# Optimization experiments

Hardware: AMD Instinct MI355X
Metric: run time of the kernel (lower is better)

Reference implementation:

```python
import jax, jax.numpy as jnp
import numpy as np

E = 8        # num_experts
K = 2        # top_k
B, S, D, H = 4, 2048, 1024, 2048  # batch, seq, input_size, hidden_size (GLU -> 2H fan-out)


def act_quant(x):
    # per-token 8-bit absmax quantization (BitNet style)
    scale = 127.0 / jnp.clip(jnp.max(jnp.abs(x), axis=-1, keepdims=True), 1e-5)
    return jnp.clip(jnp.round(x * scale), -128, 127) / scale


def weight_quant(w):
    # per-(expert)-tensor 1.58-bit quantization to {-1,0,1}/scale
    scale = 1.0 / jnp.clip(jnp.mean(jnp.abs(w)), 1e-5)
    return jnp.clip(jnp.round(w * scale), -1, 1) / scale


def ste(x, q):
    # straight-through estimator: forward uses q, backward passes grad of x
    return x + jax.lax.stop_gradient(q - x)


def setup_inputs() -> dict:
    key = jax.random.key(0)
    k0, k1, k2, k3 = jax.random.split(key, 4)
    x = jax.random.normal(k0, (B, S, D), jnp.float32)
    w_gate = jax.random.normal(k1, (D, E), jnp.float32) * 0.02   # router (no bias)
    w_in = jax.random.normal(k2, (E, 2 * H, D), jnp.float32) * 0.02   # ParallelExperts1_58b input_linear [E, out, in]
    w_out = jax.random.normal(k3, (E, D, H), jnp.float32) * 0.02      # output_linear [E, out, in]
    bias = jnp.zeros((D,), jnp.float32)
    return {"x": x, "w_gate": w_gate, "w_in": w_in, "w_out": w_out, "bias": bias}


def reference(x, w_gate, w_in, w_out, bias):
    bsz, length, d = x.shape
    xf = x.reshape(-1, d)                               # [N, D]
    logits = xf @ w_gate                                # [N, E]
    top_logits, top_idx = jax.lax.top_k(logits, K)      # [N, K]
    gates = jax.nn.softmax(top_logits, axis=-1)         # [N, K]

    # load-balancing aux loss (switch loss + z-loss), training-mode router loss
    probs = jax.nn.softmax(logits, axis=-1)
    onehot = jax.nn.one_hot(top_idx, E, dtype=logits.dtype).sum(axis=1)  # [N, E]
    freq = onehot.sum(axis=0)
    p = probs.sum(axis=0)
    switchloss = E * jnp.sum((p / jnp.sum(p)) * (freq / jnp.sum(freq)))
    zloss = jnp.sum(jax.nn.logsumexp(logits, axis=-1) ** 2) / xf.shape[0]
    loss = switchloss + 0.1 * zloss

    # STE-quantized activations and per-expert ternary weights
    xq = ste(xf, act_quant(xf))                          # [N, D]
    win_q = jax.vmap(lambda w: ste(w, weight_quant(w)))(w_in)    # [E, 2H, D]
    wout_q = jax.vmap(lambda w: ste(w, weight_quant(w)))(w_out)  # [E, D, H]

    # dense expert loop (E is small/static); gates zero-out non-routed tokens,
    # equivalent to the gather/grouped-GEMM/index_add pipeline in the original.
    y = jnp.zeros_like(xf)
    for e in range(E):
        gate_e = jnp.sum(jnp.where(top_idx == e, gates, 0.0), axis=1)  # [N]
        h = xq @ win_q[e].T                              # [N, 2H]
        h1, g = jnp.split(h, 2, axis=-1)
        h = jax.nn.silu(h1) * g                          # GLU
        hq = ste(h, act_quant(h))
        y = y + gate_e[:, None] * (hq @ wout_q[e].T)     # [N, D]

    y = y.reshape(bsz, length, d) + bias
    return y, loss
```

## Files before the change

kernel.cpp:

```cpp
#include <hip/hip_runtime.h>
#include <math.h>

typedef __attribute__((ext_vector_type(4))) int   i32x4;
typedef __attribute__((ext_vector_type(4))) float f32x4;
typedef __attribute__((ext_vector_type(8))) unsigned short u16x8;

#define NTOK   8192
#define DIMD   1024
#define HID    2048
#define NEXP   8
#define NPAIR  16384

#define XQ_OFF      0L
#define WQIN_OFF    8388608L
#define WQOUT_OFF   41943040L
#define HQ_OFF      58720256L
#define GLU_OFF     92274688L
#define XREC_OFF    226492416L
#define GATE_OFF    226525184L
#define HREC_OFF    226590720L
#define HABS_OFF    226656256L
#define TLIST_OFF   226721792L
#define CNT_OFF     226983936L
#define PSUM_OFF    226983968L
#define ZSUM_OFF    226984000L
#define PART_OFF    226984032L
#define WRECIN_OFF  226988128L
#define WRECOUT_OFF 226988160L
#define WSCLIN_OFF  226988192L
#define WSCLOUT_OFF 226988224L

__device__ __forceinline__ int clampi(int v, int lo, int hi){ return v<lo?lo:(v>hi?hi:v); }

__device__ __forceinline__ unsigned packq(f32x4 v, float s, int lo, int hi){
  int q0 = clampi((int)rintf(v.x*s), lo, hi);
  int q1 = clampi((int)rintf(v.y*s), lo, hi);
  int q2 = clampi((int)rintf(v.z*s), lo, hi);
  int q3 = clampi((int)rintf(v.w*s), lo, hi);
  return (unsigned)((q0&255)|((q1&255)<<8)|((q2&255)<<16)|((q3&255)<<24));
}

__device__ __forceinline__ unsigned short f2bf(float f){
  unsigned u = __float_as_uint(f);
  u += 0x7fffu + ((u >> 16) & 1u);
  return (unsigned short)(u >> 16);
}
__device__ __forceinline__ float bf2f(unsigned short b){
  return __uint_as_float(((unsigned)b) << 16);
}

__global__ void k_init(unsigned* __restrict__ habs, int* __restrict__ cnts,
                       float* __restrict__ psum, float* __restrict__ zsum){
  int i = blockIdx.x*blockDim.x + threadIdx.x;
  if (i < NPAIR) habs[i] = 0u;
  if (i < 8){ cnts[i]=0; psum[i]=0.f; }
  if (i == 8) zsum[0]=0.f;
}

__global__ __launch_bounds__(1024) void k_router(
    const float* __restrict__ x, const float* __restrict__ wg,
    signed char* __restrict__ xq, float* __restrict__ xrec,
    float* __restrict__ gatep, int* __restrict__ tlist, int* __restrict__ cnts,
    float* __restrict__ psum, float* __restrict__ zsum)
{
  __shared__ float ls_p[8]; __shared__ float ls_z[1];
  __shared__ int ls_c[8];  __shared__ int ls_b[8];
  int tid = threadIdx.x;
  if (tid<8){ ls_p[tid]=0.f; ls_c[tid]=0; }
  if (tid==8) ls_z[0]=0.f;
  __syncthreads();
  int wave = tid>>6, lane = tid&63;
  int tok = blockIdx.x*16 + wave;

  const f32x4* x4 = (const f32x4*)(x + (long)tok*DIMD) + lane*4;
  f32x4 xv[4];
  #pragma unroll
  for (int j=0;j<4;++j) xv[j] = x4[j];

  float amax = 0.f;
  float lg[8] = {0,0,0,0,0,0,0,0};
  const f32x4* wg4 = (const f32x4*)wg;
  #pragma unroll
  for (int j=0;j<16;++j){
    float xd = xv[j>>2][j&3];
    amax = fmaxf(amax, fabsf(xd));
    int d = lane*16 + j;
    f32x4 w0 = wg4[d*2], w1 = wg4[d*2+1];
    lg[0]+=xd*w0.x; lg[1]+=xd*w0.y; lg[2]+=xd*w0.z; lg[3]+=xd*w0.w;
    lg[4]+=xd*w1.x; lg[5]+=xd*w1.y; lg[6]+=xd*w1.z; lg[7]+=xd*w1.w;
  }
  for (int m=1;m<64;m<<=1){
    amax = fmaxf(amax, __shfl_xor(amax, m));
    #pragma unroll
    for (int e=0;e<8;++e) lg[e] += __shfl_xor(lg[e], m);
  }
  float cm = fmaxf(amax, 1e-5f);
  float sx = 127.f/cm;
  unsigned p0 = packq(xv[0], sx, -128, 127);
  unsigned p1 = packq(xv[1], sx, -128, 127);
  unsigned p2 = packq(xv[2], sx, -128, 127);
  unsigned p3 = packq(xv[3], sx, -128, 127);
  i32x4 pk; pk.x=(int)p0; pk.y=(int)p1; pk.z=(int)p2; pk.w=(int)p3;
  *(i32x4*)(xq + (long)tok*DIMD + lane*16) = pk;

  int e1=0, e2=0, s1=0, s2=0;
  if (lane==0){
    xrec[tok] = cm*(1.f/127.f);
    e1 = 0;
    for (int e=1;e<8;++e) if (lg[e] > lg[e1]) e1 = e;
    e2 = (e1==0)?1:0;
    for (int e=0;e<8;++e) if (e!=e1 && lg[e] > lg[e2]) e2 = e;
    float t = expf(lg[e2]-lg[e1]);
    gatep[tok*2]   = 1.f/(1.f+t);
    gatep[tok*2+1] = t/(1.f+t);
    float mx = lg[e1], sum = 0.f, pr[8];
    #pragma unroll
    for (int e=0;e<8;++e){ pr[e] = expf(lg[e]-mx); sum += pr[e]; }
    float inv = 1.f/sum;
    #pragma unroll
    for (int e=0;e<8;++e) atomicAdd(&ls_p[e], pr[e]*inv);
    float lse = mx + logf(sum);
    atomicAdd(&ls_z[0], lse*lse);
    s1 = atomicAdd(&ls_c[e1], 1);
    s2 = atomicAdd(&ls_c[e2], 1);
  }
  __syncthreads();
  if (tid<8) ls_b[tid] = atomicAdd(&cnts[tid], ls_c[tid]);
  __syncthreads();
  if (lane==0){
    tlist[e1*NTOK + ls_b[e1] + s1] = tok*2;
    tlist[e2*NTOK + ls_b[e2] + s2] = tok*2 + 1;
  }
  if (tid<8)  atomicAdd(&psum[tid], ls_p[tid]);
  if (tid==8) atomicAdd(zsum, ls_z[0]);
}

__global__ void k_wabs(const float* __restrict__ w_in, const float* __restrict__ w_out,
                       float* __restrict__ part){
  int b = blockIdx.x, tid = threadIdx.x;
  const float* base = (b < 512) ? (w_in + (long)b*65536) : (w_out + (long)(b-512)*65536);
  const f32x4* p4 = (const f32x4*)base;
  float s = 0.f;
  for (int i = tid; i < 16384; i += 256){
    f32x4 v = p4[i];
    s += fabsf(v.x)+fabsf(v.y)+fabsf(v.z)+fabsf(v.w);
  }
  __shared__ float red[256];
  red[tid] = s; __syncthreads();
  for (int off=128; off; off>>=1){ if (tid<off) red[tid]+=red[tid+off]; __syncthreads(); }
  if (tid==0) part[b] = red[0];
}

__global__ void k_wmean(const float* __restrict__ part,
                        float* __restrict__ wrec_in, float* __restrict__ wrec_out,
                        float* __restrict__ wscl_in, float* __restrict__ wscl_out){
  int t = threadIdx.x;
  if (t < 8){
    float s = 0.f;
    for (int i=0;i<64;++i) s += part[t*64+i];
    float cmm = fmaxf(s/4194304.f, 1e-5f);
    wrec_in[t] = cmm; wscl_in[t] = 1.f/cmm;
  } else if (t < 16){
    int e = t-8; float s = 0.f;
    for (int i=0;i<32;++i) s += part[512 + e*32 + i];
    float cmm = fmaxf(s/2097152.f, 1e-5f);
    wrec_out[e] = cmm; wscl_out[e] = 1.f/cmm;
  }
}

__global__ void k_packw(const float* __restrict__ w, i32x4* __restrict__ wq,
                        const float* __restrict__ wscl, int COLS, int K, int KB,
                        long chunksPerE){
  long t = (long)blockIdx.x*blockDim.x + threadIdx.x;
  int e = (int)(t / chunksPerE);
  long r = t - (long)e*chunksPerE;
  int lane = (int)(r & 63);
  long fb = r >> 6;
  int kb = (int)(fb % KB);
  int cb = (int)(fb / KB);
  int col = cb*16 + (lane & 15);
  int k0  = kb*64 + (lane >> 4)*16;
  const f32x4* src = (const f32x4*)(w + ((long)e*COLS + col)*K + k0);
  float s = wscl[e];
  f32x4 v0 = src[0], v1 = src[1], v2 = src[2], v3 = src[3];
  i32x4 o;
  o.x = (int)packq(v0, s, -1, 1);
  o.y = (int)packq(v1, s, -1, 1);
  o.z = (int)packq(v2, s, -1, 1);
  o.w = (int)packq(v3, s, -1, 1);
  wq[t] = o;
}

#define MFMA8(A, B, ACC) \
  { _Pragma("unroll") for (int c=0;c<8;++c) \
      ACC[c] = __builtin_amdgcn_mfma_i32_16x16x64_i8(A, B[c], ACC[c], 0,0,0); }

__global__ __launch_bounds__(256) void k_gemm1(
    const signed char* __restrict__ xq, const signed char* __restrict__ wqin,
    const int* __restrict__ tlist, const int* __restrict__ cnts,
    const float* __restrict__ xrec, const float* __restrict__ wrec_in,
    unsigned short* __restrict__ glu, unsigned* __restrict__ habs)
{
  const int e = blockIdx.y;
  const int cnt = cnts[e];
  const int slot = blockIdx.x >> 5;
  const int row0 = slot << 7;
  if (row0 >= cnt) return;
  const int ctile = blockIdx.x & 31;
  const int wave = threadIdx.x >> 6, lane = threadIdx.x & 63;
  const int l15 = lane & 15, lhi = lane >> 4;
  const int rbase = row0 + wave*32;
  const int* tl = tlist + e*NTOK;

  const i32x4* aptr[2];
  #pragma unroll
  for (int rt=0; rt<2; ++rt){
    int r = rbase + rt*16 + l15;
    int pr = tl[min(r, cnt-1)];
    aptr[rt] = (const i32x4*)(xq + (long)(pr>>1)*DIMD + lhi*16);
  }
  const i32x4* bbase[8];
  {
    const signed char* wp = wqin + (long)e*4194304 + (long)lane*16;
    #pragma unroll
    for (int c=0;c<8;++c){
      int cb_c = (c<4) ? (ctile*4 + c) : (128 + ctile*4 + (c-4));
      bbase[c] = (const i32x4*)(wp + (long)cb_c*16384);
    }
  }
  i32x4 acc0[8] = {}, acc1[8] = {};
  i32x4 e_a0 = aptr[0][0],  e_a1 = aptr[1][0];
  i32x4 o_a0 = aptr[0][4],  o_a1 = aptr[1][4];
  i32x4 e_b[8], o_b[8];
  #pragma unroll
  for (int c=0;c<8;++c){ e_b[c] = bbase[c][0]; o_b[c] = bbase[c][64]; }
  #pragma unroll 1
  for (int kb=0; kb<14; kb+=2){
    MFMA8(e_a0, e_b, acc0); MFMA8(e_a1, e_b, acc1);
    e_a0 = aptr[0][(kb+2)*4]; e_a1 = aptr[1][(kb+2)*4];
    #pragma unroll
    for (int c=0;c<8;++c) e_b[c] = bbase[c][(kb+2)*64];
    MFMA8(o_a0, o_b, acc0); MFMA8(o_a1, o_b, acc1);
    o_a0 = aptr[0][(kb+3)*4]; o_a1 = aptr[1][(kb+3)*4];
    #pragma unroll
    for (int c=0;c<8;++c) o_b[c] = bbase[c][(kb+3)*64];
  }
  MFMA8(e_a0, e_b, acc0); MFMA8(e_a1, e_b, acc1);
  MFMA8(o_a0, o_b, acc0); MFMA8(o_a1, o_b, acc1);

  const float wr = wrec_in[e];
  #pragma unroll
  for (int rt=0; rt<2; ++rt){
    #pragma unroll
    for (int i=0; i<4; ++i){
      int r = rbase + rt*16 + lhi*4 + i;
      bool valid = (r < cnt);
      int pr = valid ? tl[r] : 0;
      float dq = xrec[pr>>1] * wr;
      float m = 0.f;
      #pragma unroll
      for (int c=0;c<4;++c){
        float h1 = (float)(rt==0 ? acc0[c][i]   : acc1[c][i])   * dq;
        float gg = (float)(rt==0 ? acc0[c+4][i] : acc1[c+4][i]) * dq;
        float sil = h1 / (1.f + expf(-h1));
        float v = sil * gg;
        m = fmaxf(m, fabsf(v));
        if (valid) glu[(long)pr*HID + ctile*64 + c*16 + l15] = f2bf(v);
      }
      #pragma unroll
      for (int mm=1; mm<16; mm<<=1) m = fmaxf(m, __shfl_xor(m, mm));
      if (valid && l15==0) atomicMax(habs + pr, __float_as_uint(m));
    }
  }
}

__global__ void k_quanth(const unsigned short* __restrict__ glu, const unsigned* __restrict__ habs,
                         signed char* __restrict__ hq, float* __restrict__ hrec){
  int p = blockIdx.x, t = threadIdx.x;
  float am = __uint_as_float(habs[p]);
  float cmm = fmaxf(am, 1e-5f);
  if (t==0) hrec[p] = cmm*(1.f/127.f);
  float s = 127.f/cmm;
  u16x8 v = ((const u16x8*)(glu + (long)p*HID))[t];
  f32x4 f0, f1;
  f0.x=bf2f(v[0]); f0.y=bf2f(v[1]); f0.z=bf2f(v[2]); f0.w=bf2f(v[3]);
  f1.x=bf2f(v[4]); f1.y=bf2f(v[5]); f1.z=bf2f(v[6]); f1.w=bf2f(v[7]);
  uint2 u; u.x = packq(f0, s, -128, 127); u.y = packq(f1, s, -128, 127);
  ((uint2*)(hq + (long)p*HID))[t] = u;
}

__global__ __launch_bounds__(256) void k_gemm2(
    const signed char* __restrict__ hq, const signed char* __restrict__ wqout,
    const int* __restrict__ tlist, const int* __restrict__ cnts,
    const float* __restrict__ hrec, const float* __restrict__ gatep,
    const float* __restrict__ wrec_out, float* __restrict__ pout)
{
  const int e = blockIdx.y;
  const int cnt = cnts[e];
  const int slot = blockIdx.x >> 3;
  const int row0 = slot << 7;
  if (row0 >= cnt) return;
  const int ctile = blockIdx.x & 7;
  const int dcol0 = ctile*128;
  const int wave = threadIdx.x >> 6, lane = threadIdx.x & 63;
  const int l15 = lane & 15, lhi = lane >> 4;
  const int rbase = row0 + wave*32;
  const int* tl = tlist + e*NTOK;

  const i32x4* aptr[2];
  #pragma unroll
  for (int rt=0; rt<2; ++rt){
    int r = rbase + rt*16 + l15;
    int pr = tl[min(r, cnt-1)];
    aptr[rt] = (const i32x4*)(hq + (long)pr*HID + lhi*16);
  }
  const i32x4* bbase[8];
  {
    const signed char* wp = wqout + (long)e*2097152 + (long)lane*16;
    #pragma unroll
    for (int c=0;c<8;++c){
      int cb_c = ctile*8 + c;
      bbase[c] = (const i32x4*)(wp + (long)cb_c*32768);
    }
  }
  i32x4 acc0[8] = {}, acc1[8] = {};
  i32x4 e_a0 = aptr[0][0],  e_a1 = aptr[1][0];
  i32x4 o_a0 = aptr[0][4],  o_a1 = aptr[1][4];
  i32x4 e_b[8], o_b[8];
  #pragma unroll
  for (int c=0;c<8;++c){ e_b[c] = bbase[c][0]; o_b[c] = bbase[c][64]; }
  #pragma unroll 1
  for (int kb=0; kb<30; kb+=2){
    MFMA8(e_a0, e_b, acc0); MFMA8(e_a1, e_b, acc1);
    e_a0 = aptr[0][(kb+2)*4]; e_a1 = aptr[1][(kb+2)*4];
    #pragma unroll
    for (int c=0;c<8;++c) e_b[c] = bbase[c][(kb+2)*64];
    MFMA8(o_a0, o_b, acc0); MFMA8(o_a1, o_b, acc1);
    o_a0 = aptr[0][(kb+3)*4]; o_a1 = aptr[1][(kb+3)*4];
    #pragma unroll
    for (int c=0;c<8;++c) o_b[c] = bbase[c][(kb+3)*64];
  }
  MFMA8(e_a0, e_b, acc0); MFMA8(e_a1, e_b, acc1);
  MFMA8(o_a0, o_b, acc0); MFMA8(o_a1, o_b, acc1);

  const float wr = wrec_out[e];
  #pragma unroll
  for (int rt=0; rt<2; ++rt){
    #pragma unroll
    for (int i=0; i<4; ++i){
      int r = rbase + rt*16 + lhi*4 + i;
      if (r >= cnt) continue;
      int pr = tl[r];
      float f = gatep[pr] * hrec[pr] * wr;
      #pragma unroll
      for (int c=0;c<8;++c)
        pout[(long)pr*DIMD + dcol0 + c*16 + l15] = (float)(rt==0 ? acc0[c][i] : acc1[c][i]) * f;
    }
  }
}

__global__ void k_combine(const float* __restrict__ pout, const float* __restrict__ bias,
                          float* __restrict__ y){
  long idx = (long)blockIdx.x*blockDim.x + threadIdx.x;
  int tok = (int)(idx >> 8);
  int c4  = (int)(idx & 255);
  f32x4 b  = ((const f32x4*)bias)[c4];
  const f32x4* p = (const f32x4*)(pout + (long)tok*2*DIMD);
  f32x4 r = b + p[c4] + p[256 + c4];
  ((f32x4*)(y + (long)tok*DIMD))[c4] = r;
}

__global__ void k_loss(const int* __restrict__ cnts, const float* __restrict__ psum,
                       const float* __restrict__ zsum, float* __restrict__ out){
  if (threadIdx.x==0 && blockIdx.x==0){
    float sp=0.f, sf=0.f, sw=0.f;
    for (int e=0;e<8;++e){
      float f = (float)cnts[e];
      sp += psum[e]; sf += f; sw += psum[e]*f;
    }
    float loss = 8.f*sw/(sp*sf) + 0.1f*zsum[0]/(float)NTOK;
    out[(long)NTOK*DIMD] = loss;
  }
}

extern "C" void kernel_launch(void* const* d_in, const int* in_sizes, int n_in,
                              void* d_out, int out_size, void* d_ws, size_t ws_size,
                              hipStream_t stream){
  const float* x     = (const float*)d_in[0];
  const float* wg    = (const float*)d_in[1];
  const float* w_in  = (const float*)d_in[2];
  const float* w_out = (const float*)d_in[3];
  const float* bias  = (const float*)d_in[4];
  float* y = (float*)d_out;
  char* ws = (char*)d_ws;

  signed char* xq    = (signed char*)(ws + XQ_OFF);
  signed char* wqin  = (signed char*)(ws + WQIN_OFF);
  signed char* wqout = (signed char*)(ws + WQOUT_OFF);
  signed char* hq    = (signed char*)(ws + HQ_OFF);
  unsigned short* glu = (unsigned short*)(ws + GLU_OFF);
  float* pout  = (float*)(ws + GLU_OFF);
  float* xrec  = (float*)(ws + XREC_OFF);
  float* gatep = (float*)(ws + GATE_OFF);
  float* hrec  = (float*)(ws + HREC_OFF);
  unsigned* habs = (unsigned*)(ws + HABS_OFF);
  int* tlist = (int*)(ws + TLIST_OFF);
  int* cnts  = (int*)(ws + CNT_OFF);
  float* psum = (float*)(ws + PSUM_OFF);
  float* zsum = (float*)(ws + ZSUM_OFF);
  float* part = (float*)(ws + PART_OFF);
  float* wrec_in  = (float*)(ws + WRECIN_OFF);
  float* wrec_out = (float*)(ws + WRECOUT_OFF);
  float* wscl_in  = (float*)(ws + WSCLIN_OFF);
  float* wscl_out = (float*)(ws + WSCLOUT_OFF);

  k_init  <<<64, 256, 0, stream>>>(habs, cnts, psum, zsum);
  k_router<<<512, 1024, 0, stream>>>(x, wg, xq, xrec, gatep, tlist, cnts, psum, zsum);
  k_wabs  <<<768, 256, 0, stream>>>(w_in, w_out, part);
  k_wmean <<<1, 64, 0, stream>>>(part, wrec_in, wrec_out, wscl_in, wscl_out);
  k_packw <<<8192, 256, 0, stream>>>(w_in,  (i32x4*)wqin,  wscl_in,  4096, 1024, 16, 262144L);
  k_packw <<<4096, 256, 0, stream>>>(w_out, (i32x4*)wqout, wscl_out, 1024, 2048, 32, 131072L);
  k_gemm1 <<<dim3(2048, 8), 256, 0, stream>>>(xq, wqin, tlist, cnts, xrec, wrec_in, glu, habs);
  k_quanth<<<NPAIR, 256, 0, stream>>>(glu, habs, hq, hrec);
  k_gemm2 <<<dim3(512, 8), 256, 0, stream>>>(hq, wqout, tlist, cnts, hrec, gatep, wrec_out, pout);
  k_combine<<<8192, 256, 0, stream>>>(pout, bias, y);
  k_loss  <<<1, 64, 0, stream>>>(cnts, psum, zsum, y);
}
```

Baseline: 479.2 us.

## Switch expert GEMMs to 32x32x32 int8 MFMA with grid-stride job scheduling

Replaces the 16x16x64 int8 MFMA tiles in both expert GEMMs with 32x32x32 int8 MFMA using four 16-wide accumulators per wave. The weight packing layout changes to match the new operand fragment shape. Both GEMMs move from a 2D grid with many early-exit blocks to a persistent-style 1D grid where each block loops over jobs interleaved across experts. The goal is higher MFMA throughput per instruction, fewer redundant operand loads, and less launch waste from empty tiles. The epilogue is reworked for the new accumulator row mapping, including a wider shuffle reduction for the row absmax.

```diff
diff --git a/kernel.cpp b/kernel.cpp
--- a/kernel.cpp
+++ b/kernel.cpp
@@ -1,9 +1,10 @@
 #include <hip/hip_runtime.h>
 #include <math.h>
 
-typedef __attribute__((ext_vector_type(4))) int   i32x4;
-typedef __attribute__((ext_vector_type(4))) float f32x4;
-typedef __attribute__((ext_vector_type(8))) unsigned short u16x8;
+typedef __attribute__((ext_vector_type(4)))  int   i32x4;
+typedef __attribute__((ext_vector_type(16))) int   i32x16;
+typedef __attribute__((ext_vector_type(4)))  float f32x4;
+typedef __attribute__((ext_vector_type(8)))  unsigned short u16x8;
 
 #define NTOK   8192
 #define DIMD   1024
@@ -178,8 +179,8 @@
   long fb = r >> 6;
   int kb = (int)(fb % KB);
   int cb = (int)(fb / KB);
-  int col = cb*16 + (lane & 15);
-  int k0  = kb*64 + (lane >> 4)*16;
+  int col = cb*32 + (lane & 31);
+  int k0  = kb*32 + (lane >> 5)*16;
   const f32x4* src = (const f32x4*)(w + ((long)e*COLS + col)*K + k0);
   float s = wscl[e];
   f32x4 v0 = src[0], v1 = src[1], v2 = src[2], v3 = src[3];
@@ -191,9 +192,11 @@
   wq[t] = o;
 }
 
-#define MFMA8(A, B, ACC) \
-  { _Pragma("unroll") for (int c=0;c<8;++c) \
-      ACC[c] = __builtin_amdgcn_mfma_i32_16x16x64_i8(A, B[c], ACC[c], 0,0,0); }
+#define MFMA32(A, B0, B1, B2, B3) \
+  acc0 = __builtin_amdgcn_mfma_i32_32x32x32_i8(A, B0, acc0, 0,0,0); \
+  acc1 = __builtin_amdgcn_mfma_i32_32x32x32_i8(A, B1, acc1, 0,0,0); \
+  acc2 = __builtin_amdgcn_mfma_i32_32x32x32_i8(A, B2, acc2, 0,0,0); \
+  acc3 = __builtin_amdgcn_mfma_i32_32x32x32_i8(A, B3, acc3, 0,0,0);
 
 __global__ __launch_bounds__(256) void k_gemm1(
     const signed char* __restrict__ xq, const signed char* __restrict__ wqin,
@@ -201,75 +204,64 @@
     const float* __restrict__ xrec, const float* __restrict__ wrec_in,
     unsigned short* __restrict__ glu, unsigned* __restrict__ habs)
 {
-  const int e = blockIdx.y;
-  const int cnt = cnts[e];
-  const int slot = blockIdx.x >> 5;
-  const int row0 = slot << 7;
-  if (row0 >= cnt) return;
-  const int ctile = blockIdx.x & 31;
   const int wave = threadIdx.x >> 6, lane = threadIdx.x & 63;
-  const int l15 = lane & 15, lhi = lane >> 4;
-  const int rbase = row0 + wave*32;
-  const int* tl = tlist + e*NTOK;
-
-  const i32x4* aptr[2];
-  #pragma unroll
-  for (int rt=0; rt<2; ++rt){
-    int r = rbase + rt*16 + l15;
-    int pr = tl[min(r, cnt-1)];
-    aptr[rt] = (const i32x4*)(xq + (long)(pr>>1)*DIMD + lhi*16);
-  }
-  const i32x4* bbase[8];
-  {
+  const int l31 = lane & 31, lhi = lane >> 5;
+  for (int job = blockIdx.x; job < 16384; job += 4096){
+    const int ctile = job & 31;
+    const int e = (job >> 5) & 7;
+    const int slot = job >> 8;
+    const int cnt = cnts[e];
+    const int row0 = slot << 7;
+    if (row0 >= cnt) continue;
+
+    const int* tl = tlist + e*NTOK;
+    const int rbase = row0 + wave*32;
+    const int ar = tl[min(rbase + l31, cnt-1)];
+    const i32x4* ap = (const i32x4*)(xq + (long)(ar>>1)*DIMD + lhi*16);
     const signed char* wp = wqin + (long)e*4194304 + (long)lane*16;
+    const i32x4* bp0 = (const i32x4*)(wp + (long)(ctile*2     )*32768);
+    const i32x4* bp1 = (const i32x4*)(wp + (long)(ctile*2 +  1)*32768);
+    const i32x4* bp2 = (const i32x4*)(wp + (long)(ctile*2 + 64)*32768);
+    const i32x4* bp3 = (const i32x4*)(wp + (long)(ctile*2 + 65)*32768);
+
+    i32x16 acc0 = (i32x16)0, acc1 = (i32x16)0, acc2 = (i32x16)0, acc3 = (i32x16)0;
+    i32x4 ea = ap[0], oa = ap[2];
+    i32x4 eb0 = bp0[0],  eb1 = bp1[0],  eb2 = bp2[0],  eb3 = bp3[0];
+    i32x4 ob0 = bp0[64], ob1 = bp1[64], ob2 = bp2[64], ob3 = bp3[64];
+    #pragma unroll 1
+    for (int kb=0; kb<30; kb+=2){
+      ap += 4; bp0 += 128; bp1 += 128; bp2 += 128; bp3 += 128;
+      MFMA32(ea, eb0, eb1, eb2, eb3);
+      ea = ap[0];
+      eb0 = bp0[0]; eb1 = bp1[0]; eb2 = bp2[0]; eb3 = bp3[0];
+      MFMA32(oa, ob0, ob1, ob2, ob3);
+      oa = ap[2];
+      ob0 = bp0[64]; ob1 = bp1[64]; ob2 = bp2[64]; ob3 = bp3[64];
+    }
+    MFMA32(ea, eb0, eb1, eb2, eb3);
+    MFMA32(oa, ob0, ob1, ob2, ob3);
+
+    const float wr = wrec_in[e];
     #pragma unroll
-    for (int c=0;c<8;++c){
-      int cb_c = (c<4) ? (ctile*4 + c) : (128 + ctile*4 + (c-4));
-      bbase[c] = (const i32x4*)(wp + (long)cb_c*16384);
-    }
-  }
-  i32x4 acc0[8] = {}, acc1[8] = {};
-  i32x4 e_a0 = aptr[0][0],  e_a1 = aptr[1][0];
-  i32x4 o_a0 = aptr[0][4],  o_a1 = aptr[1][4];
-  i32x4 e_b[8], o_b[8];
-  #pragma unroll
-  for (int c=0;c<8;++c){ e_b[c] = bbase[c][0]; o_b[c] = bbase[c][64]; }
-  #pragma unroll 1
-  for (int kb=0; kb<14; kb+=2){
-    MFMA8(e_a0, e_b, acc0); MFMA8(e_a1, e_b, acc1);
-    e_a0 = aptr[0][(kb+2)*4]; e_a1 = aptr[1][(kb+2)*4];
-    #pragma unroll
-    for (int c=0;c<8;++c) e_b[c] = bbase[c][(kb+2)*64];
-    MFMA8(o_a0, o_b, acc0); MFMA8(o_a1, o_b, acc1);
-    o_a0 = aptr[0][(kb+3)*4]; o_a1 = aptr[1][(kb+3)*4];
-    #pragma unroll
-    for (int c=0;c<8;++c) o_b[c] = bbase[c][(kb+3)*64];
-  }
-  MFMA8(e_a0, e_b, acc0); MFMA8(e_a1, e_b, acc1);
-  MFMA8(o_a0, o_b, acc0); MFMA8(o_a1, o_b, acc1);
-
-  const float wr = wrec_in[e];
-  #pragma unroll
-  for (int rt=0; rt<2; ++rt){
-    #pragma unroll
-    for (int i=0; i<4; ++i){
-      int r = rbase + rt*16 + lhi*4 + i;
+    for (int g=0; g<16; ++g){
+      int rl = (g&3) + 8*(g>>2) + 4*lhi;
+      int r  = rbase + rl;
       bool valid = (r < cnt);
       int pr = valid ? tl[r] : 0;
       float dq = xrec[pr>>1] * wr;
-      float m = 0.f;
-      #pragma unroll
-      for (int c=0;c<4;++c){
-        float h1 = (float)(rt==0 ? acc0[c][i]   : acc1[c][i])   * dq;
-        float gg = (float)(rt==0 ? acc0[c+4][i] : acc1[c+4][i]) * dq;
-        float sil = h1 / (1.f + expf(-h1));
-        float v = sil * gg;
-        m = fmaxf(m, fabsf(v));
-        if (valid) glu[(long)pr*HID + ctile*64 + c*16 + l15] = f2bf(v);
+      float h1a = (float)acc0[g]*dq, gga = (float)acc2[g]*dq;
+      float h1b = (float)acc1[g]*dq, ggb = (float)acc3[g]*dq;
+      float v0 = h1a/(1.f+expf(-h1a))*gga;
+      float v1 = h1b/(1.f+expf(-h1b))*ggb;
+      float m = fmaxf(fabsf(v0), fabsf(v1));
+      if (valid){
+        long base = (long)pr*HID + ctile*64;
+        glu[base + l31]      = f2bf(v0);
+        glu[base + 32 + l31] = f2bf(v1);
       }
       #pragma unroll
-      for (int mm=1; mm<16; mm<<=1) m = fmaxf(m, __shfl_xor(m, mm));
-      if (valid && l15==0) atomicMax(habs + pr, __float_as_uint(m));
+      for (int mm=1; mm<32; mm<<=1) m = fmaxf(m, __shfl_xor(m, mm));
+      if (valid && l31==0) atomicMax(habs + pr, __float_as_uint(m));
     }
   }
 }
@@ -295,66 +287,56 @@
     const float* __restrict__ hrec, const float* __restrict__ gatep,
     const float* __restrict__ wrec_out, float* __restrict__ pout)
 {
-  const int e = blockIdx.y;
-  const int cnt = cnts[e];
-  const int slot = blockIdx.x >> 3;
-  const int row0 = slot << 7;
-  if (row0 >= cnt) return;
-  const int ctile = blockIdx.x & 7;
-  const int dcol0 = ctile*128;
   const int wave = threadIdx.x >> 6, lane = threadIdx.x & 63;
-  const int l15 = lane & 15, lhi = lane >> 4;
-  const int rbase = row0 + wave*32;
-  const int* tl = tlist + e*NTOK;
-
-  const i32x4* aptr[2];
-  #pragma unroll
-  for (int rt=0; rt<2; ++rt){
-    int r = rbase + rt*16 + l15;
-    int pr = tl[min(r, cnt-1)];
-    aptr[rt] = (const i32x4*)(hq + (long)pr*HID + lhi*16);
-  }
-  const i32x4* bbase[8];
-  {
+  const int l31 = lane & 31, lhi = lane >> 5;
+  for (int job = blockIdx.x; job < 4096; job += 1024){
+    const int ctile = job & 7;
+    const int e = (job >> 3) & 7;
+    const int slot = job >> 6;
+    const int cnt = cnts[e];
+    const int row0 = slot << 7;
+    if (row0 >= cnt) continue;
+
+    const int* tl = tlist + e*NTOK;
+    const int rbase = row0 + wave*32;
+    const int ar = tl[min(rbase + l31, cnt-1)];
+    const i32x4* ap = (const i32x4*)(hq + (long)ar*HID + lhi*16);
     const signed char* wp = wqout + (long)e*2097152 + (long)lane*16;
+    const i32x4* bp0 = (const i32x4*)(wp + (long)(ctile*4    )*65536);
+    const i32x4* bp1 = (const i32x4*)(wp + (long)(ctile*4 + 1)*65536);
+    const i32x4* bp2 = (const i32x4*)(wp + (long)(ctile*4 + 2)*65536);
+    const i32x4* bp3 = (const i32x4*)(wp + (long)(ctile*4 + 3)*65536);
+
+    i32x16 acc0 = (i32x16)0, acc1 = (i32x16)0, acc2 = (i32x16)0, acc3 = (i32x16)0;
+    i32x4 ea = ap[0], oa = ap[2];
+    i32x4 eb0 = bp0[0],  eb1 = bp1[0],  eb2 = bp2[0],  eb3 = bp3[0];
+    i32x4 ob0 = bp0[64], ob1 = bp1[64], ob2 = bp2[64], ob3 = bp3[64];
+    #pragma unroll 1
+    for (int kb=0; kb<62; kb+=2){
+      ap += 4; bp0 += 128; bp1 += 128; bp2 += 128; bp3 += 128;
+      MFMA32(ea, eb0, eb1, eb2, eb3);
+      ea = ap[0];
+      eb0 = bp0[0]; eb1 = bp1[0]; eb2 = bp2[0]; eb3 = bp3[0];
+      MFMA32(oa, ob0, ob1, ob2, ob3);
+      oa = ap[2];
+      ob0 = bp0[64]; ob1 = bp1[64]; ob2 = bp2[64]; ob3 = bp3[64];
+    }
+    MFMA32(ea, eb0, eb1, eb2, eb3);
+    MFMA32(oa, ob0, ob1, ob2, ob3);
+
+    const float wr = wrec_out[e];
     #pragma unroll
-    for (int c=0;c<8;++c){
-      int cb_c = ctile*8 + c;
-      bbase[c] = (const i32x4*)(wp + (long)cb_c*32768);
-    }
-  }
-  i32x4 acc0[8] = {}, acc1[8] = {};
-  i32x4 e_a0 = aptr[0][0],  e_a1 = aptr[1][0];
-  i32x4 o_a0 = aptr[0][4],  o_a1 = aptr[1][4];
-  i32x4 e_b[8], o_b[8];
-  #pragma unroll
-  for (int c=0;c<8;++c){ e_b[c] = bbase[c][0]; o_b[c] = bbase[c][64]; }
-  #pragma unroll 1
-  for (int kb=0; kb<30; kb+=2){
-    MFMA8(e_a0, e_b, acc0); MFMA8(e_a1, e_b, acc1);
-    e_a0 = aptr[0][(kb+2)*4]; e_a1 = aptr[1][(kb+2)*4];
-    #pragma unroll
-    for (int c=0;c<8;++c) e_b[c] = bbase[c][(kb+2)*64];
-    MFMA8(o_a0, o_b, acc0); MFMA8(o_a1, o_b, acc1);
-    o_a0 = aptr[0][(kb+3)*4]; o_a1 = aptr[1][(kb+3)*4];
-    #pragma unroll
-    for (int c=0;c<8;++c) o_b[c] = bbase[c][(kb+3)*64];
-  }
-  MFMA8(e_a0, e_b, acc0); MFMA8(e_a1, e_b, acc1);
-  MFMA8(o_a0, o_b, acc0); MFMA8(o_a1, o_b, acc1);
-
-  const float wr = wrec_out[e];
-  #pragma unroll
-  for (int rt=0; rt<2; ++rt){
-    #pragma unroll
-    for (int i=0; i<4; ++i){
-      int r = rbase + rt*16 + lhi*4 + i;
+    for (int g=0; g<16; ++g){
+      int rl = (g&3) + 8*(g>>2) + 4*lhi;
+      int r  = rbase + rl;
       if (r >= cnt) continue;
       int pr = tl[r];
       float f = gatep[pr] * hrec[pr] * wr;
-      #pragma unroll
-      for (int c=0;c<8;++c)
-        pout[(long)pr*DIMD + dcol0 + c*16 + l15] = (float)(rt==0 ? acc0[c][i] : acc1[c][i]) * f;
+      long base = (long)pr*DIMD + ctile*128;
+      pout[base + l31]      = (float)acc0[g]*f;
+      pout[base + 32 + l31] = (float)acc1[g]*f;
+      pout[base + 64 + l31] = (float)acc2[g]*f;
+      pout[base + 96 + l31] = (float)acc3[g]*f;
     }
   }
 }
@@ -418,11 +400,11 @@
   k_router<<<512, 1024, 0, stream>>>(x, wg, xq, xrec, gatep, tlist, cnts, psum, zsum);
   k_wabs  <<<768, 256, 0, stream>>>(w_in, w_out, part);
   k_wmean <<<1, 64, 0, stream>>>(part, wrec_in, wrec_out, wscl_in, wscl_out);
-  k_packw <<<8192, 256, 0, stream>>>(w_in,  (i32x4*)wqin,  wscl_in,  4096, 1024, 16, 262144L);
-  k_packw <<<4096, 256, 0, stream>>>(w_out, (i32x4*)wqout, wscl_out, 1024, 2048, 32, 131072L);
-  k_gemm1 <<<dim3(2048, 8), 256, 0, stream>>>(xq, wqin, tlist, cnts, xrec, wrec_in, glu, habs);
+  k_packw <<<8192, 256, 0, stream>>>(w_in,  (i32x4*)wqin,  wscl_in,  4096, 1024, 32, 262144L);
+  k_packw <<<4096, 256, 0, stream>>>(w_out, (i32x4*)wqout, wscl_out, 1024, 2048, 64, 131072L);
+  k_gemm1 <<<4096, 256, 0, stream>>>(xq, wqin, tlist, cnts, xrec, wrec_in, glu, habs);
   k_quanth<<<NPAIR, 256, 0, stream>>>(glu, habs, hq, hrec);
-  k_gemm2 <<<dim3(512, 8), 256, 0, stream>>>(hq, wqout, tlist, cnts, hrec, gatep, wrec_out, pout);
+  k_gemm2 <<<1024, 256, 0, stream>>>(hq, wqout, tlist, cnts, hrec, gatep, wrec_out, pout);
   k_combine<<<8192, 256, 0, stream>>>(pout, bias, y);
   k_loss  <<<1, 64, 0, stream>>>(cnts, psum, zsum, y);
 }
```

Result: slower. 522.4 us (+9.0%).
